# Performance work log

Measured on AMD Instinct MI355X. Metric: run time of the kernel, lower is better.

## Reference

```python
import jax, jax.numpy as jnp
import numpy as np

N_ENT = 100000


def setup_inputs() -> dict:
    key = jax.random.key(0)
    ks = jax.random.split(key, 8)
    d, R, E = 128, 8, 600000
    scale = 1.0 / np.sqrt(d)  # xavier-ish so relu activations stay sane
    return {
        "entity_emb": jax.random.normal(ks[0], (N_ENT, d), dtype=jnp.float32),
        "w1": jax.random.normal(ks[1], (R, d, d), dtype=jnp.float32) * scale,
        "sl1": jax.random.normal(ks[2], (d, d), dtype=jnp.float32) * scale,
        "b1": jnp.zeros((d,), dtype=jnp.float32),
        "w2": jax.random.normal(ks[3], (R, d, d), dtype=jnp.float32) * scale,
        "sl2": jax.random.normal(ks[4], (d, d), dtype=jnp.float32) * scale,
        "b2": jnp.zeros((d,), dtype=jnp.float32),
        "edge_index": jax.random.randint(ks[5], (2, E), 0, N_ENT, dtype=jnp.int64),
        "edge_type": jax.random.randint(ks[6], (E,), 0, R, dtype=jnp.int64),
    }


def _rgcn_layer(x, W, SW, b, src, dst, rel):
    # Transform all nodes by every relation weight once ([R,N,d]),
    # then gather the per-edge message x[src] @ W[rel] and scatter-add to dst.
    xt = jnp.einsum('nd,rde->rne', x, W)          # [R, N, d]
    msg = xt[rel, src]                            # [E, d]
    agg = jax.ops.segment_sum(msg, dst, num_segments=x.shape[0])  # [N, d]
    return jax.nn.relu(agg + x @ SW + b)


def reference(entity_emb, w1, sl1, b1, w2, sl2, b2, edge_index, edge_type):
    src, dst = edge_index[0], edge_index[1]
    x = _rgcn_layer(entity_emb, w1, sl1, b1, src, dst, edge_type)
    x = _rgcn_layer(x, w2, sl2, b2, src, dst, edge_type)
    return x
```

## Files before the change

### kernel.cpp

```cpp
#include <hip/hip_runtime.h>

#define D 128
#define BM 128
#define NREL 8
#define SCAN_BLOCKS 782
#define MPAD (SCAN_BLOCKS * 1024)

typedef __attribute__((ext_vector_type(8))) short short8;
typedef __attribute__((ext_vector_type(8))) unsigned short ushort8;
typedef __attribute__((ext_vector_type(4))) float f32x4;

typedef const void __attribute__((address_space(1))) gvoid_t;
typedef void __attribute__((address_space(3))) lvoid_t;

__device__ inline unsigned short f2bf(float f) {
  unsigned u = __builtin_bit_cast(unsigned, f);
  u += 0x7FFFu + ((u >> 16) & 1u);
  return (unsigned short)(u >> 16);
}

__device__ inline void gload16(const void* g, void* l) {
  __builtin_amdgcn_global_load_lds((gvoid_t*)g, (lvoid_t*)l, 16, 0, 0);
}

__global__ __launch_bounds__(256) void cvt_x(const float* __restrict__ x,
                                             unsigned short* __restrict__ dst,
                                             long total ) {
  long i = (long)blockIdx.x * 256 + threadIdx.x;
  if (i >= total) return;
  float4 v = reinterpret_cast<const float4*>(x)[i];
  unsigned lo = (unsigned)f2bf(v.x) | ((unsigned)f2bf(v.y) << 16);
  unsigned hi = (unsigned)f2bf(v.z) | ((unsigned)f2bf(v.w) << 16);
  reinterpret_cast<uint2*>(dst)[i] = make_uint2(lo, hi);
}

__global__ __launch_bounds__(256) void wcvt(const float* __restrict__ W,
                                            const float* __restrict__ SW,
                                            unsigned short* __restrict__ Btr) {
  int idx = blockIdx.x * 256 + threadIdx.x;
  if (idx >= 9 * D * D) return;
  int r = idx >> 14;
  int rem = idx & 16383;
  int col = rem >> 7;
  int k = rem & 127;
  float v = (r < NREL) ? W[((r * D) + k) * D + col] : SW[k * D + col];
  Btr[idx] = f2bf(v);
}

__global__ __launch_bounds__(256) void hist_kernel(const int* __restrict__ dst,
                                                   const int* __restrict__ rel,
                                                   int* __restrict__ counts, int E) {
  int e = blockIdx.x * 256 + threadIdx.x;
  if (e >= E) return;
  atomicAdd(&counts[(dst[e] << 3) | rel[e]], 1);
}

__global__ __launch_bounds__(256) void scan1(const int* __restrict__ in,
                                             int* __restrict__ out,
                                             int* __restrict__ bsum) {
  __shared__ int tmp[256];
  int t = threadIdx.x;
  long base = (long)blockIdx.x * 1024 + t * 4;
  int v[4];
  int s = 0;
#pragma unroll
  for (int j = 0; j < 4; ++j) {
    v[j] = in[base + j];
    s += v[j];
  }
  tmp[t] = s;
  __syncthreads();
  for (int off = 1; off < 256; off <<= 1) {
    int x = (t >= off) ? tmp[t - off] : 0;
    __syncthreads();
    tmp[t] += x;
    __syncthreads();
  }
  int run = tmp[t] - s;
  if (t == 255) bsum[blockIdx.x] = tmp[255];
#pragma unroll
  for (int j = 0; j < 4; ++j) {
    out[base + j] = run;
    run += v[j];
  }
}

__global__ __launch_bounds__(1024) void scan_top(int* __restrict__ bsum, int nb) {
  __shared__ int tmp[1024];
  int t = threadIdx.x;
  int v = (t < nb) ? bsum[t] : 0;
  tmp[t] = v;
  __syncthreads();
  for (int off = 1; off < 1024; off <<= 1) {
    int x = (t >= off) ? tmp[t - off] : 0;
    __syncthreads();
    tmp[t] += x;
    __syncthreads();
  }
  if (t < nb) bsum[t] = tmp[t] - v;
}

__global__ __launch_bounds__(256) void scan_add(int* __restrict__ starts,
                                                int* __restrict__ cursor,
                                                const int* __restrict__ bsum) {
  long base = (long)blockIdx.x * 1024 + threadIdx.x * 4;
  int add = bsum[blockIdx.x];
#pragma unroll
  for (int j = 0; j < 4; ++j) {
    int v = starts[base + j] + add;
    starts[base + j] = v;
    cursor[base + j] = v;
  }
}

__global__ __launch_bounds__(256) void reorder(const int* __restrict__ src,
                                               const int* __restrict__ dst,
                                               const int* __restrict__ rel,
                                               int* __restrict__ cursor,
                                               int* __restrict__ esort, int E) {
  int e = blockIdx.x * 256 + threadIdx.x;
  if (e >= E) return;
  int key = (dst[e] << 3) | rel[e];
  int pos = atomicAdd(&cursor[key], 1);
  esort[pos] = src[e];
}

__global__ __launch_bounds__(256) void fused_layer(
    const unsigned short* __restrict__ xb, const int* __restrict__ starts,
    const int* __restrict__ esort, const unsigned short* __restrict__ Btr,
    const float* __restrict__ bias, unsigned short* __restrict__ xout_b,
    float* __restrict__ outf, int N) {
  __shared__ char As[32768];
  __shared__ char Bs[32768];

  const int tid = threadIdx.x;
  const int wave = tid >> 6, lane = tid & 63;
  const int wm = wave >> 1, wn = wave & 1;
  const int l15 = lane & 15, lq = lane >> 4;
  const int row0 = blockIdx.x * BM;

  f32x4 acc[4][4];
#pragma unroll
  for (int m = 0; m < 4; ++m)
#pragma unroll
    for (int n = 0; n < 4; ++n)
#pragma unroll
      for (int q = 0; q < 4; ++q) acc[m][n][q] = 0.f;

  for (int r = 0; r < 9; ++r) {
    const unsigned short* Bsrc = Btr + r * (D * D);
#pragma unroll
    for (int i = 0; i < 8; ++i) {
      int o = i * 4096 + tid * 16;
      int row = o >> 8, b = o & 255;
      int sb = b ^ ((row & 7) << 4);
      gload16(Bsrc + row * D + (sb >> 1), Bs + o);
    }
    if (r < NREL) {
#pragma unroll
      for (int half = 0; half < 2; ++half) {
        int lr = half * 64 + (tid >> 2);
        int cb = tid & 3;
        int dstn = row0 + lr;
        float a[32];
#pragma unroll
        for (int j = 0; j < 32; ++j) a[j] = 0.f;
        if (dstn < N) {
          int e0 = starts[(dstn << 3) + r];
          int e1 = starts[(dstn << 3) + r + 1];
          for (int e = e0; e < e1; ++e) {
            int s = esort[e];
            const ushort8* p =
                reinterpret_cast<const ushort8*>(xb + (size_t)s * D + cb * 32);
#pragma unroll
            for (int j = 0; j < 4; ++j) {
              ushort8 v = p[j];
#pragma unroll
              for (int k = 0; k < 8; ++k)
                a[j * 8 + k] +=
                    __builtin_bit_cast(float, (unsigned)v[k] << 16);
            }
          }
        }
#pragma unroll
        for (int j = 0; j < 4; ++j) {
          short8 w;
#pragma unroll
          for (int k = 0; k < 8; ++k) w[k] = (short)f2bf(a[j * 8 + k]);
          int b = (cb * 64 + j * 16) ^ ((lr & 7) << 4);
          *reinterpret_cast<short8*>(As + lr * 256 + b) = w;
        }
      }
    } else {
#pragma unroll
      for (int i = 0; i < 8; ++i) {
        int o = i * 4096 + tid * 16;
        int row = o >> 8, b = o & 255;
        int grow = row0 + row;
        if (grow >= N) grow = N - 1;
        int sb = b ^ ((row & 7) << 4);
        gload16(xb + (size_t)grow * D + (sb >> 1), As + o);
      }
    }
    __syncthreads();
#pragma unroll
    for (int kh = 0; kh < 2; ++kh) {
      short8 af[4][2], bfr[4][2];
#pragma unroll
      for (int m = 0; m < 4; ++m)
#pragma unroll
        for (int k2 = 0; k2 < 2; ++k2) {
          int rr = wm * 64 + m * 16 + l15;
          int b = ((kh * 2 + k2) * 64 + lq * 16) ^ ((rr & 7) << 4);
          af[m][k2] = *reinterpret_cast<const short8*>(As + rr * 256 + b);
        }
#pragma unroll
      for (int n = 0; n < 4; ++n)
#pragma unroll
        for (int k2 = 0; k2 < 2; ++k2) {
          int rr = wn * 64 + n * 16 + l15;
          int b = ((kh * 2 + k2) * 64 + lq * 16) ^ ((rr & 7) << 4);
          bfr[n][k2] = *reinterpret_cast<const short8*>(Bs + rr * 256 + b);
        }
#pragma unroll
      for (int m = 0; m < 4; ++m)
#pragma unroll
        for (int n = 0; n < 4; ++n) {
          acc[m][n] = __builtin_amdgcn_mfma_f32_16x16x32_bf16(
              af[m][0], bfr[n][0], acc[m][n], 0, 0, 0);
          acc[m][n] = __builtin_amdgcn_mfma_f32_16x16x32_bf16(
              af[m][1], bfr[n][1], acc[m][n], 0, 0, 0);
        }
    }
    __syncthreads();
  }

#pragma unroll
  for (int n = 0; n < 4; ++n) {
    int col = wn * 64 + n * 16 + l15;
    float bv = bias[col];
#pragma unroll
    for (int m = 0; m < 4; ++m) {
      int rbase = row0 + wm * 64 + m * 16 + lq * 4;
#pragma unroll
      for (int q = 0; q < 4; ++q) {
        int row = rbase + q;
        if (row < N) {
          float v = fmaxf(acc[m][n][q] + bv, 0.f);
          if (outf)
            outf[(size_t)row * D + col] = v;
          else
            xout_b[(size_t)row * D + col] = f2bf(v);
        }
      }
    }
  }
}

extern "C" void kernel_launch(void* const* d_in, const int* in_sizes, int n_in,
                              void* d_out, int out_size, void* d_ws, size_t ws_size,
                              hipStream_t stream) {
  const float* emb = (const float*)d_in[0];
  const float* W1 = (const float*)d_in[1];
  const float* SL1 = (const float*)d_in[2];
  const float* B1 = (const float*)d_in[3];
  const float* W2 = (const float*)d_in[4];
  const float* SL2 = (const float*)d_in[5];
  const float* B2 = (const float*)d_in[6];
  const int* eidx = (const int*)d_in[7];
  const int* etyp = (const int*)d_in[8];
  const int N = in_sizes[0] / D;
  const int E = in_sizes[8];
  const int* srcp = eidx;
  const int* dstp = eidx + E;
  float* outp = (float*)d_out;

  char* w = (char*)d_ws;
  unsigned short* xb0 = (unsigned short*)w;
  unsigned short* xb1 = xb0 + (size_t)N * D;
  unsigned short* Btr1 = xb1 + (size_t)N * D;
  unsigned short* Btr2 = Btr1 + 9 * D * D;
  int* counts = (int*)(Btr2 + 9 * D * D);
  int* starts = counts + MPAD;
  int* cursor = starts + MPAD;
  int* bsum = cursor + MPAD;
  int* esort = bsum + 1024;

  const int eb = (E + 255) / 256;
  const int gm_blocks = (N + BM - 1) / BM;

  hipMemsetAsync(counts, 0, (size_t)MPAD * 4, stream);
  cvt_x<<<(int)(((long)N * 32 + 255) / 256), 256, 0, stream>>>(emb, xb0,
                                                               (long)N * 32);
  wcvt<<<(9 * D * D + 255) / 256, 256, 0, stream>>>(W1, SL1, Btr1);
  wcvt<<<(9 * D * D + 255) / 256, 256, 0, stream>>>(W2, SL2, Btr2);
  hist_kernel<<<eb, 256, 0, stream>>>(dstp, etyp, counts, E);
  scan1<<<SCAN_BLOCKS, 256, 0, stream>>>(counts, starts, bsum);
  scan_top<<<1, 1024, 0, stream>>>(bsum, SCAN_BLOCKS);
  scan_add<<<SCAN_BLOCKS, 256, 0, stream>>>(starts, cursor, bsum);
  reorder<<<eb, 256, 0, stream>>>(srcp, dstp, etyp, cursor, esort, E);

  fused_layer<<<gm_blocks, 256, 0, stream>>>(xb0, starts, esort, Btr1, B1, xb1,
                                             nullptr, N);
  fused_layer<<<gm_blocks, 256, 0, stream>>>(xb1, starts, esort, Btr2, B2,
                                             nullptr, outp, N);
}
```

Baseline: 365.3 us.

## Aggregate edges via LDS bf16 atomic adds with relation-major CSR and preswizzled weights

Sorting keys change from dst-major to relation-major so each block's edges for one relation form a single contiguous range. Edges are stored as (src,dst) pairs and are processed 64 at a time across all threads. Each edge's features are accumulated directly into the LDS A tile with ds_pk_add_bf16, instead of one thread per dst row looping serially over its edges in fp32 registers. This is meant to balance work across threads and remove per-row serial loops. Weights are pre-swizzled in one merged conversion kernel so B tiles load linearly, and the swizzle widens to 16 rows. The cost is that accumulation happens in bf16, which loses precision, plus LDS atomic contention when many edges share a destination row.

```diff
diff --git a/kernel.cpp b/kernel.cpp
--- a/kernel.cpp
+++ b/kernel.cpp
@@ -7,7 +7,6 @@
 #define MPAD (SCAN_BLOCKS * 1024)
 
 typedef __attribute__((ext_vector_type(8))) short short8;
-typedef __attribute__((ext_vector_type(8))) unsigned short ushort8;
 typedef __attribute__((ext_vector_type(4))) float f32x4;
 
 typedef const void __attribute__((address_space(1))) gvoid_t;
@@ -21,6 +20,11 @@
 
 __device__ inline void gload16(const void* g, void* l) {
   __builtin_amdgcn_global_load_lds((gvoid_t*)g, (lvoid_t*)l, 16, 0, 0);
+}
+
+__device__ inline void ds_pk_add(void* lptr, unsigned data) {
+  asm volatile("ds_pk_add_bf16 %0, %1" ::"v"((lvoid_t*)lptr), "v"(data)
+               : "memory");
 }
 
 __global__ __launch_bounds__(256) void cvt_x(const float* __restrict__ x,
@@ -34,25 +38,33 @@
   reinterpret_cast<uint2*>(dst)[i] = make_uint2(lo, hi);
 }
 
-__global__ __launch_bounds__(256) void wcvt(const float* __restrict__ W,
-                                            const float* __restrict__ SW,
+__global__ __launch_bounds__(256) void wcvt(const float* __restrict__ W1,
+                                            const float* __restrict__ SL1,
+                                            const float* __restrict__ W2,
+                                            const float* __restrict__ SL2,
                                             unsigned short* __restrict__ Btr) {
   int idx = blockIdx.x * 256 + threadIdx.x;
-  if (idx >= 9 * D * D) return;
-  int r = idx >> 14;
-  int rem = idx & 16383;
-  int col = rem >> 7;
-  int k = rem & 127;
-  float v = (r < NREL) ? W[((r * D) + k) * D + col] : SW[k * D + col];
+  if (idx >= 2 * 9 * D * D) return;
+  int l = idx >= 9 * D * D;
+  int t = idx - l * 9 * D * D;
+  int r = t >> 14;
+  int rem = t & 16383;
+  int c = rem >> 7;
+  int pb = rem & 127;
+  int k = pb ^ ((c & 15) << 3);
+  const float* W = l ? W2 : W1;
+  const float* SL = l ? SL2 : SL1;
+  float v = (r < NREL) ? W[((r * D) + k) * D + c] : SL[k * D + c];
   Btr[idx] = f2bf(v);
 }
 
 __global__ __launch_bounds__(256) void hist_kernel(const int* __restrict__ dst,
                                                    const int* __restrict__ rel,
-                                                   int* __restrict__ counts, int E) {
+                                                   int* __restrict__ counts,
+                                                   int E, int N) {
   int e = blockIdx.x * 256 + threadIdx.x;
   if (e >= E) return;
-  atomicAdd(&counts[(dst[e] << 3) | rel[e]], 1);
+  atomicAdd(&counts[rel[e] * N + dst[e]], 1);
 }
 
 __global__ __launch_bounds__(256) void scan1(const int* __restrict__ in,
@@ -117,17 +129,17 @@
                                                const int* __restrict__ dst,
                                                const int* __restrict__ rel,
                                                int* __restrict__ cursor,
-                                               int* __restrict__ esort, int E) {
+                                               int2* __restrict__ es, int E,
+                                               int N) {
   int e = blockIdx.x * 256 + threadIdx.x;
   if (e >= E) return;
-  int key = (dst[e] << 3) | rel[e];
-  int pos = atomicAdd(&cursor[key], 1);
-  esort[pos] = src[e];
+  int pos = atomicAdd(&cursor[rel[e] * N + dst[e]], 1);
+  es[pos] = make_int2(src[e], dst[e]);
 }
 
 __global__ __launch_bounds__(256) void fused_layer(
     const unsigned short* __restrict__ xb, const int* __restrict__ starts,
-    const int* __restrict__ esort, const unsigned short* __restrict__ Btr,
+    const int2* __restrict__ es, const unsigned short* __restrict__ Btr,
     const float* __restrict__ bias, unsigned short* __restrict__ xout_b,
     float* __restrict__ outf, int N) {
   __shared__ char As[32768];
@@ -138,6 +150,8 @@
   const int wm = wave >> 1, wn = wave & 1;
   const int l15 = lane & 15, lq = lane >> 4;
   const int row0 = blockIdx.x * BM;
+  const int rowend = (row0 + BM < N) ? (row0 + BM) : N;
+  const int eg = tid >> 2, cb = tid & 3;
 
   f32x4 acc[4][4];
 #pragma unroll
@@ -148,47 +162,40 @@
       for (int q = 0; q < 4; ++q) acc[m][n][q] = 0.f;
 
   for (int r = 0; r < 9; ++r) {
-    const unsigned short* Bsrc = Btr + r * (D * D);
+    __syncthreads();
+    const char* bsrc = reinterpret_cast<const char*>(Btr) + r * 32768;
 #pragma unroll
     for (int i = 0; i < 8; ++i) {
       int o = i * 4096 + tid * 16;
-      int row = o >> 8, b = o & 255;
-      int sb = b ^ ((row & 7) << 4);
-      gload16(Bsrc + row * D + (sb >> 1), Bs + o);
+      gload16(bsrc + o, Bs + o);
     }
     if (r < NREL) {
 #pragma unroll
-      for (int half = 0; half < 2; ++half) {
-        int lr = half * 64 + (tid >> 2);
-        int cb = tid & 3;
-        int dstn = row0 + lr;
-        float a[32];
-#pragma unroll
-        for (int j = 0; j < 32; ++j) a[j] = 0.f;
-        if (dstn < N) {
-          int e0 = starts[(dstn << 3) + r];
-          int e1 = starts[(dstn << 3) + r + 1];
-          for (int e = e0; e < e1; ++e) {
-            int s = esort[e];
-            const ushort8* p =
-                reinterpret_cast<const ushort8*>(xb + (size_t)s * D + cb * 32);
-#pragma unroll
-            for (int j = 0; j < 4; ++j) {
-              ushort8 v = p[j];
-#pragma unroll
-              for (int k = 0; k < 8; ++k)
-                a[j * 8 + k] +=
-                    __builtin_bit_cast(float, (unsigned)v[k] << 16);
-            }
+      for (int i = 0; i < 8; ++i)
+        *reinterpret_cast<int4*>(As + i * 4096 + tid * 16) =
+            make_int4(0, 0, 0, 0);
+      __syncthreads();
+      int e0 = starts[r * N + row0];
+      int e1 = starts[r * N + rowend];
+      for (int eb = e0; eb < e1; eb += 64) {
+        int e = eb + eg;
+        if (e < e1) {
+          int2 sd = es[e];
+          const uint4* p =
+              reinterpret_cast<const uint4*>(xb + (size_t)sd.x * D) + cb * 4;
+          int dstl = sd.y - row0;
+          int swz = (dstl & 15) << 4;
+          char* rowp = As + dstl * 256;
+          uint4 u0 = p[0], u1 = p[1], u2 = p[2], u3 = p[3];
+#pragma unroll
+          for (int j = 0; j < 4; ++j) {
+            uint4 u = (j == 0) ? u0 : (j == 1) ? u1 : (j == 2) ? u2 : u3;
+            char* bp = rowp + (((cb * 64 + j * 16)) ^ swz);
+            ds_pk_add(bp + 0, u.x);
+            ds_pk_add(bp + 4, u.y);
+            ds_pk_add(bp + 8, u.z);
+            ds_pk_add(bp + 12, u.w);
           }
-        }
-#pragma unroll
-        for (int j = 0; j < 4; ++j) {
-          short8 w;
-#pragma unroll
-          for (int k = 0; k < 8; ++k) w[k] = (short)f2bf(a[j * 8 + k]);
-          int b = (cb * 64 + j * 16) ^ ((lr & 7) << 4);
-          *reinterpret_cast<short8*>(As + lr * 256 + b) = w;
         }
       }
     } else {
@@ -198,8 +205,9 @@
         int row = o >> 8, b = o & 255;
         int grow = row0 + row;
         if (grow >= N) grow = N - 1;
-        int sb = b ^ ((row & 7) << 4);
-        gload16(xb + (size_t)grow * D + (sb >> 1), As + o);
+        int sb = b ^ ((row & 15) << 4);
+        gload16(reinterpret_cast<const char*>(xb + (size_t)grow * D) + sb,
+                As + o);
       }
     }
     __syncthreads();
@@ -211,7 +219,7 @@
 #pragma unroll
         for (int k2 = 0; k2 < 2; ++k2) {
           int rr = wm * 64 + m * 16 + l15;
-          int b = ((kh * 2 + k2) * 64 + lq * 16) ^ ((rr & 7) << 4);
+          int b = ((kh * 2 + k2) * 64 + lq * 16) ^ ((rr & 15) << 4);
           af[m][k2] = *reinterpret_cast<const short8*>(As + rr * 256 + b);
         }
 #pragma unroll
@@ -219,7 +227,7 @@
 #pragma unroll
         for (int k2 = 0; k2 < 2; ++k2) {
           int rr = wn * 64 + n * 16 + l15;
-          int b = ((kh * 2 + k2) * 64 + lq * 16) ^ ((rr & 7) << 4);
+          int b = ((kh * 2 + k2) * 64 + lq * 16) ^ ((rr & 15) << 4);
           bfr[n][k2] = *reinterpret_cast<const short8*>(Bs + rr * 256 + b);
         }
 #pragma unroll
@@ -232,7 +240,6 @@
               af[m][1], bfr[n][1], acc[m][n], 0, 0, 0);
         }
     }
-    __syncthreads();
   }
 
 #pragma unroll
@@ -278,13 +285,12 @@
   char* w = (char*)d_ws;
   unsigned short* xb0 = (unsigned short*)w;
   unsigned short* xb1 = xb0 + (size_t)N * D;
-  unsigned short* Btr1 = xb1 + (size_t)N * D;
-  unsigned short* Btr2 = Btr1 + 9 * D * D;
-  int* counts = (int*)(Btr2 + 9 * D * D);
+  unsigned short* Btr = xb1 + (size_t)N * D;
+  int* counts = (int*)(Btr + 2 * 9 * D * D);
   int* starts = counts + MPAD;
   int* cursor = starts + MPAD;
   int* bsum = cursor + MPAD;
-  int* esort = bsum + 1024;
+  int2* es = (int2*)(bsum + 1024);
 
   const int eb = (E + 255) / 256;
   const int gm_blocks = (N + BM - 1) / BM;
@@ -292,16 +298,15 @@
   hipMemsetAsync(counts, 0, (size_t)MPAD * 4, stream);
   cvt_x<<<(int)(((long)N * 32 + 255) / 256), 256, 0, stream>>>(emb, xb0,
                                                                (long)N * 32);
-  wcvt<<<(9 * D * D + 255) / 256, 256, 0, stream>>>(W1, SL1, Btr1);
-  wcvt<<<(9 * D * D + 255) / 256, 256, 0, stream>>>(W2, SL2, Btr2);
-  hist_kernel<<<eb, 256, 0, stream>>>(dstp, etyp, counts, E);
+  wcvt<<<(2 * 9 * D * D + 255) / 256, 256, 0, stream>>>(W1, SL1, W2, SL2, Btr);
+  hist_kernel<<<eb, 256, 0, stream>>>(dstp, etyp, counts, E, N);
   scan1<<<SCAN_BLOCKS, 256, 0, stream>>>(counts, starts, bsum);
   scan_top<<<1, 1024, 0, stream>>>(bsum, SCAN_BLOCKS);
   scan_add<<<SCAN_BLOCKS, 256, 0, stream>>>(starts, cursor, bsum);
-  reorder<<<eb, 256, 0, stream>>>(srcp, dstp, etyp, cursor, esort, E);
-
-  fused_layer<<<gm_blocks, 256, 0, stream>>>(xb0, starts, esort, Btr1, B1, xb1,
+  reorder<<<eb, 256, 0, stream>>>(srcp, dstp, etyp, cursor, es, E, N);
+
+  fused_layer<<<gm_blocks, 256, 0, stream>>>(xb0, starts, es, Btr, B1, xb1,
                                              nullptr, N);
-  fused_layer<<<gm_blocks, 256, 0, stream>>>(xb1, starts, esort, Btr2, B2,
-                                             nullptr, outp, N);
-}
+  fused_layer<<<gm_blocks, 256, 0, stream>>>(
+      xb1, starts, es, Btr + 9 * D * D, B2, nullptr, outp, N);
+}
```

New measurement: 705.8 us. 93.2% more time.
